# Kernel optimization log

Measured on AMD Instinct MI355X. Metric: run time of the kernel, lower is better.

## Reference

```python
import jax, jax.numpy as jnp
import numpy as np

# Sizes (see init_kwargs / shape_source)
N = 65536      # total points
B = 8          # batch elements
PPB = N // B   # points per batch element (8192, divisible by WS -> no padding)
D = 256        # d_model
H = 8          # nhead
DH = D // H
L = 4          # num_layers
FF = 2048      # torch TransformerEncoderLayer default dim_feedforward
RES = 128      # resolution (coordinate range / embedding table size)
BITS = 7       # ceil(log2(RES)); higher bits of morton loop are zero
WS = 128       # window_size
EPS = 1e-5     # LayerNorm eps


def setup_inputs() -> dict:
    key = jax.random.key(0)
    ks = jax.random.split(key, 16)
    s = 0.02
    batch_col = (jnp.arange(N) // PPB).astype(jnp.int32)
    xyz = jax.random.randint(ks[0], (N, 3), 0, RES, dtype=jnp.int32)
    coords = jnp.concatenate([batch_col[:, None], xyz], axis=1)
    features = jax.random.normal(ks[1], (N, D), jnp.float32)
    inp = {
        'coords': coords,
        'features': features,
        # learned positional embedding tables
        'pe_x': jax.random.normal(ks[2], (RES, D), jnp.float32) * s,
        'pe_y': jax.random.normal(ks[3], (RES, D), jnp.float32) * s,
        'pe_z': jax.random.normal(ks[4], (RES, D), jnp.float32) * s,
        'pe_s': jax.random.normal(ks[5], (RES, D), jnp.float32) * s,
        # stacked transformer encoder layer params (torch post-norm layer)
        'Wqkv': jax.random.normal(ks[6], (L, 3 * D, D), jnp.float32) * s,
        'bqkv': jnp.zeros((L, 3 * D), jnp.float32),
        'Wo': jax.random.normal(ks[7], (L, D, D), jnp.float32) * s,
        'bo': jnp.zeros((L, D), jnp.float32),
        'W1': jax.random.normal(ks[8], (L, FF, D), jnp.float32) * s,
        'b1': jnp.zeros((L, FF), jnp.float32),
        'W2': jax.random.normal(ks[9], (L, D, FF), jnp.float32) * s,
        'b2': jnp.zeros((L, D), jnp.float32),
        'g1': jnp.ones((L, D), jnp.float32),
        'be1': jnp.zeros((L, D), jnp.float32),
        'g2': jnp.ones((L, D), jnp.float32),
        'be2': jnp.zeros((L, D), jnp.float32),
    }
    return inp


def _morton_key(coords):
    # interleave bits of x,y,z (z lowest), prefix with batch index so batch order is preserved
    x, y, z = coords[:, 1], coords[:, 2], coords[:, 3]
    m = jnp.zeros_like(x)
    for i in range(BITS):
        m = m | (((x >> i) & 1) << (3 * i + 2)) \
              | (((y >> i) & 1) << (3 * i + 1)) \
              | (((z >> i) & 1) << (3 * i))
    return coords[:, 0] * (1 << (3 * BITS)) + m


def _ln(x, g, b):
    mu = jnp.mean(x, axis=-1, keepdims=True)
    var = jnp.mean(jnp.square(x - mu), axis=-1, keepdims=True)
    return (x - mu) * jax.lax.rsqrt(var + EPS) * g + b


def _encoder(x, params):
    # x: [Wn, WS, D]; torch TransformerEncoderLayer, post-norm, relu, no dropout (eval)
    scale = float(DH) ** -0.5

    def layer(h, p):
        Wqkv, bqkv, Wo, bo, W1, b1, W2, b2, g1, be1, g2, be2 = p
        Wn = h.shape[0]
        qkv = h @ Wqkv.T + bqkv                      # [Wn, WS, 3D]
        q, k, v = jnp.split(qkv, 3, axis=-1)
        q = q.reshape(Wn, WS, H, DH)
        k = k.reshape(Wn, WS, H, DH)
        v = v.reshape(Wn, WS, H, DH)
        att = jax.nn.softmax(jnp.einsum('wqhd,wkhd->whqk', q, k) * scale, axis=-1)
        o = jnp.einsum('whqk,wkhd->wqhd', att, v).reshape(Wn, WS, D) @ Wo.T + bo
        h = _ln(h + o, g1, be1)
        ff = jax.nn.relu(h @ W1.T + b1) @ W2.T + b2
        h = _ln(h + ff, g2, be2)
        return h, None

    x, _ = jax.lax.scan(layer, x, params)
    return x


def reference(coords, features, pe_x, pe_y, pe_z, pe_s,
              Wqkv, bqkv, Wo, bo, W1, b1, W2, b2, g1, be1, g2, be2):
    # 1) Morton sort (stable, batch-major)
    idx = jnp.argsort(_morton_key(coords))
    sc = coords[idx]
    sf = features[idx]
    # 2) learned positional encoding (stride = 1)
    pe = pe_x[sc[:, 1]] + pe_y[sc[:, 2]] + pe_z[sc[:, 3]] + pe_s[1]
    x = sf + pe
    # 3) window split: PPB % WS == 0, interval == 1 -> exact tiling, no padding
    x = x.reshape(-1, WS, D)                          # [Wn, WS, D]
    # 4) transformer encoder over windows
    x = _encoder(x, (Wqkv, bqkv, Wo, bo, W1, b1, W2, b2, g1, be1, g2, be2))
    # 5) gather back (all masks True -> simple reshape); output in sorted order
    return x.reshape(N, D)
```

## Files before the change

### kernel.cpp

```cpp
#include <hip/hip_runtime.h>

typedef unsigned int u32;
typedef unsigned short u16;

#define NPTS 65536
#define DMODEL 256
#define NHEAD 8
#define DHEAD 32
#define NLAYER 4
#define FFDIM 2048
#define WSIZE 128
#define LNEPS 1e-5f
#define RG 256

#define KSTR 36
#define VSTR 132
#define PSTR 132

typedef __attribute__((ext_vector_type(8))) short short8;
typedef __attribute__((ext_vector_type(4))) float floatx4;

__device__ __forceinline__ float bf2f(u16 v) {
    u32 u = ((u32)v) << 16;
    float f;
    __builtin_memcpy(&f, &u, 4);
    return f;
}
__device__ __forceinline__ u16 f2bf(float f) {
    u32 u;
    __builtin_memcpy(&u, &f, 4);
    u32 r = (u + 0x7fffu + ((u >> 16) & 1u)) >> 16;
    return (u16)r;
}

__device__ __forceinline__ void gl_lds16(const void* g, void* l) {
    __builtin_amdgcn_global_load_lds((const __attribute__((address_space(1))) u32*)g,
                                     (__attribute__((address_space(3))) u32*)l, 16, 0, 0);
}

__global__ __launch_bounds__(256) void morton_kernel(const int* __restrict__ coords,
                                                     u32* __restrict__ key, u32* __restrict__ val) {
    int i = blockIdx.x * 256 + threadIdx.x;
    int b = coords[4 * i + 0];
    int x = coords[4 * i + 1];
    int y = coords[4 * i + 2];
    int z = coords[4 * i + 3];
    u32 m = 0;
#pragma unroll
    for (int t = 0; t < 7; ++t) {
        m |= ((u32)((x >> t) & 1) << (3 * t + 2)) | ((u32)((y >> t) & 1) << (3 * t + 1)) |
             ((u32)((z >> t) & 1) << (3 * t));
    }
    key[i] = ((u32)b << 21) | m;
    val[i] = (u32)i;
}

__global__ __launch_bounds__(256) void hist_kernel(const u32* __restrict__ key, u32* __restrict__ ghist,
                                                   int shift) {
    __shared__ u32 h[256];
    int tid = threadIdx.x;
    h[tid] = 0;
    __syncthreads();
    u32 k = key[blockIdx.x * 256 + tid];
    atomicAdd(&h[(k >> shift) & 255u], 1u);
    __syncthreads();
    ghist[(size_t)tid * RG + blockIdx.x] = h[tid];
}

__global__ __launch_bounds__(256) void scan_up(u32* __restrict__ g, u32* __restrict__ aux) {
    __shared__ u32 wsum[4];
    int tid = threadIdx.x;
    int lane = tid & 63;
    int wave = tid >> 6;
    size_t base = (size_t)blockIdx.x * 1024 + (size_t)tid * 4;
    uint4 v = *(const uint4*)(g + base);
    u32 s = v.x + v.y + v.z + v.w;
    u32 inc = s;
#pragma unroll
    for (int off = 1; off < 64; off <<= 1) {
        u32 u = __shfl_up(inc, off, 64);
        if (lane >= off) inc += u;
    }
    if (lane == 63) wsum[wave] = inc;
    __syncthreads();
    u32 woff = 0;
    for (int w = 0; w < wave; ++w) woff += wsum[w];
    u32 excl = woff + inc - s;
    uint4 o;
    o.x = excl;
    o.y = excl + v.x;
    o.z = excl + v.x + v.y;
    o.w = excl + v.x + v.y + v.z;
    *(uint4*)(g + base) = o;
    if (tid == 255) aux[blockIdx.x] = woff + inc;
}

__global__ __launch_bounds__(256) void scatter_kernel(const u32* __restrict__ keyin, const u32* __restrict__ valin,
                                                      u32* __restrict__ keyout, u32* __restrict__ valout,
                                                      const u32* __restrict__ ghist, const u32* __restrict__ aux,
                                                      int shift) {
    __shared__ u32 whist[4][256];
    __shared__ u32 apre[64];
    int tid = threadIdx.x;
    int lane = tid & 63;
    int wave = tid >> 6;
    uint4 z = {0u, 0u, 0u, 0u};
    ((uint4*)&whist[0][0])[tid] = z;
    if (tid < 64) {
        u32 a = aux[tid];
        u32 inc = a;
#pragma unroll
        for (int off = 1; off < 64; off <<= 1) {
            u32 u = __shfl_up(inc, off, 64);
            if (lane >= off) inc += u;
        }
        apre[tid] = inc - a;
    }
    int gi = blockIdx.x * 256 + tid;
    u32 k = keyin[gi];
    u32 v = valin[gi];
    u32 b = (k >> shift) & 255u;
    __syncthreads();
    unsigned long long m = ~0ull;
#pragma unroll
    for (int bit = 0; bit < 8; ++bit) {
        unsigned long long bb = __ballot((int)((b >> bit) & 1u));
        m &= ((b >> bit) & 1u) ? bb : ~bb;
    }
    unsigned long long below = (lane == 0) ? 0ull : (m & ((1ull << lane) - 1ull));
    int rlane = __popcll(below);
    int cnt = __popcll(m);
    if (rlane == 0) whist[wave][b] = (u32)cnt;
    __syncthreads();
    u32 rank = (u32)rlane;
    for (int w = 0; w < wave; ++w) rank += whist[w][b];
    u32 e = b * (u32)RG + blockIdx.x;
    u32 dst = ghist[e] + apre[e >> 10] + rank;
    keyout[dst] = k;
    valout[dst] = v;
}

__global__ __launch_bounds__(256) void cvt_bf16_kernel(const float* __restrict__ in, u16* __restrict__ out, int n) {
    int i = blockIdx.x * 256 + threadIdx.x;
    if (i < n) out[i] = f2bf(in[i]);
}

template <bool HF32>
__global__ __launch_bounds__(256) void gather_pe_kernel(const u32* __restrict__ idx, const int* __restrict__ coords,
                                                        const float* __restrict__ feat,
                                                        const float* __restrict__ pex, const float* __restrict__ pey,
                                                        const float* __restrict__ pez, const float* __restrict__ pes,
                                                        float* __restrict__ h, u16* __restrict__ xb) {
    int row = blockIdx.x * 4 + (threadIdx.x >> 6);
    int lane = threadIdx.x & 63;
    int src = (int)idx[row];
    int cx = coords[4 * src + 1];
    int cy = coords[4 * src + 2];
    int cz = coords[4 * src + 3];
    int c = lane * 4;
    float4 f = *(const float4*)(feat + (size_t)src * DMODEL + c);
    float4 px = *(const float4*)(pex + (size_t)cx * DMODEL + c);
    float4 py = *(const float4*)(pey + (size_t)cy * DMODEL + c);
    float4 pz = *(const float4*)(pez + (size_t)cz * DMODEL + c);
    float4 ps = *(const float4*)(pes + (size_t)1 * DMODEL + c);
    float4 r;
    r.x = f.x + px.x + py.x + pz.x + ps.x;
    r.y = f.y + px.y + py.y + pz.y + ps.y;
    r.z = f.z + px.z + py.z + pz.z + ps.z;
    r.w = f.w + px.w + py.w + pz.w + ps.w;
    if (HF32) *(float4*)(h + (size_t)row * DMODEL + c) = r;
    ushort4 o;
    o.x = f2bf(r.x);
    o.y = f2bf(r.y);
    o.z = f2bf(r.z);
    o.w = f2bf(r.w);
    *(ushort4*)(xb + (size_t)row * DMODEL + c) = o;
}

template <bool RELU, bool BF16OUT>
__global__ __launch_bounds__(256, 5) void gemm_bt(const u16* __restrict__ A, const u16* __restrict__ W,
                                                  const float* __restrict__ bias, void* __restrict__ Cout,
                                                  int M, int O, int K) {
    __shared__ __align__(16) u16 lA[2 * 128 * 32];
    __shared__ __align__(16) u16 lB[2 * 128 * 32];
    const int tid = threadIdx.x;
    const int lane = tid & 63;
    const int wave = tid >> 6;
    const int wr = wave >> 1;
    const int wc = wave & 1;
    const int quad = lane >> 4;
    const int l16 = lane & 15;
    const int kz = blockIdx.z;
    const int Kpart = K / (int)gridDim.z;
    const size_t row0 = (size_t)blockIdx.x * 128;
    const size_t col0 = (size_t)blockIdx.y * 128;
    floatx4 acc[4][4] = {};

    const int r0 = tid >> 2;
    const int sg0 = (tid & 3) ^ ((r0 >> 1) & 3);
    const u16* pA = A + (row0 + r0) * (size_t)K + (size_t)kz * Kpart + (sg0 << 3);
    const u16* pW = W + (col0 + r0) * (size_t)K + (size_t)kz * Kpart + (sg0 << 3);
    const size_t rstep = (size_t)64 * K;
    const int oA = tid * 8;

    const int nt = Kpart >> 5;
    gl_lds16(pA, lA + oA);
    gl_lds16(pA + rstep, lA + oA + 2048);
    gl_lds16(pW, lB + oA);
    gl_lds16(pW + rstep, lB + oA + 2048);
    pA += 32;
    pW += 32;

    const int sx = (quad ^ ((l16 >> 1) & 3)) << 3;
    const int rdA = (wr * 64 + l16) * 32 + sx;
    const int rdB = (wc * 64 + l16) * 32 + sx;
    int buf = 0;
    for (int t = 0; t < nt; ++t) {
        if (t + 1 < nt) {
            const int nb = (buf ^ 1) * 4096;
            gl_lds16(pA, lA + nb + oA);
            gl_lds16(pA + rstep, lA + nb + oA + 2048);
            gl_lds16(pW, lB + nb + oA);
            gl_lds16(pW + rstep, lB + nb + oA + 2048);
            pA += 32;
            pW += 32;
            asm volatile("s_waitcnt vmcnt(4)" ::: "memory");
        } else {
            asm volatile("s_waitcnt vmcnt(0)" ::: "memory");
        }
        __builtin_amdgcn_s_barrier();
        const u16* la = lA + buf * 4096 + rdA;
        const u16* lb = lB + buf * 4096 + rdB;
        short8 af[4], bf[4];
#pragma unroll
        for (int r = 0; r < 4; ++r) af[r] = *(const short8*)(la + r * 512);
#pragma unroll
        for (int c = 0; c < 4; ++c) bf[c] = *(const short8*)(lb + c * 512);
#pragma unroll
        for (int r = 0; r < 4; ++r)
#pragma unroll
            for (int c = 0; c < 4; ++c)
                acc[r][c] = __builtin_amdgcn_mfma_f32_16x16x32_bf16(af[r], bf[c], acc[r][c], 0, 0, 0);
        if (t + 1 < nt) __builtin_amdgcn_s_barrier();
        buf ^= 1;
    }

    float* Cf = (float*)Cout + (size_t)kz * ((size_t)M * O);
#pragma unroll
    for (int r = 0; r < 4; ++r) {
#pragma unroll
        for (int c = 0; c < 4; ++c) {
            size_t col = col0 + wc * 64 + c * 16 + l16;
            float bv = (kz == 0) ? bias[col] : 0.f;
#pragma unroll
            for (int reg = 0; reg < 4; ++reg) {
                size_t row = row0 + wr * 64 + r * 16 + quad * 4 + reg;
                float v = acc[r][c][reg] + bv;
                if (RELU) v = fmaxf(v, 0.f);
                if (BF16OUT)
                    ((u16*)Cout)[row * O + col] = f2bf(v);
                else
                    Cf[row * O + col] = v;
            }
        }
    }
}

__global__ __launch_bounds__(128) void attn_kernel(const u16* __restrict__ qkv, u16* __restrict__ outb) {
    const int wh = blockIdx.x;
    const int w = wh >> 3;
    const int h = wh & 7;
    const int tid = threadIdx.x;
    const int wave = tid >> 6;
    const int lane = tid & 63;
    const int quad = lane >> 4;
    const int l16 = lane & 15;
    __shared__ __align__(16) u16 lK[128 * KSTR];
    __shared__ __align__(16) u16 lVt[32 * VSTR];
    __shared__ __align__(16) u16 lP[128 * PSTR];
    const u16* base = qkv + (size_t)w * WSIZE * (3 * DMODEL);

    {
        const u16* krow = base + (size_t)tid * (3 * DMODEL) + DMODEL + h * DHEAD;
        const u16* vrow = base + (size_t)tid * (3 * DMODEL) + 2 * DMODEL + h * DHEAD;
#pragma unroll
        for (int p = 0; p < 4; ++p)
            *(short8*)&lK[tid * KSTR + p * 8] = *(const short8*)(krow + p * 8);
        u16 varr[32];
#pragma unroll
        for (int p = 0; p < 4; ++p)
            *(short8*)&varr[p * 8] = *(const short8*)(vrow + p * 8);
#pragma unroll
        for (int d = 0; d < DHEAD; ++d) lVt[d * VSTR + tid] = varr[d];
    }
    short8 af[4];
#pragma unroll
    for (int mi = 0; mi < 4; ++mi)
        af[mi] = *(const short8*)(base + (size_t)(wave * 64 + mi * 16 + l16) * (3 * DMODEL) + h * DHEAD + quad * 8);
    __syncthreads();

    floatx4 acc[4][8] = {};
#pragma unroll
    for (int ni = 0; ni < 8; ++ni) {
        short8 bk = *(const short8*)&lK[(ni * 16 + l16) * KSTR + quad * 8];
#pragma unroll
        for (int mi = 0; mi < 4; ++mi)
            acc[mi][ni] = __builtin_amdgcn_mfma_f32_16x16x32_bf16(af[mi], bk, acc[mi][ni], 0, 0, 0);
    }

    const float scale = 0.17677669529663687f;
    float inv[4][4];
#pragma unroll
    for (int mi = 0; mi < 4; ++mi) {
#pragma unroll
        for (int reg = 0; reg < 4; ++reg) {
            float m = acc[mi][0][reg];
#pragma unroll
            for (int ni = 1; ni < 8; ++ni) m = fmaxf(m, acc[mi][ni][reg]);
            m = fmaxf(m, __shfl_xor(m, 1, 64));
            m = fmaxf(m, __shfl_xor(m, 2, 64));
            m = fmaxf(m, __shfl_xor(m, 4, 64));
            m = fmaxf(m, __shfl_xor(m, 8, 64));
            float e[8];
            float sum = 0.f;
#pragma unroll
            for (int ni = 0; ni < 8; ++ni) {
                e[ni] = __expf((acc[mi][ni][reg] - m) * scale);
                sum += e[ni];
            }
            sum += __shfl_xor(sum, 1, 64);
            sum += __shfl_xor(sum, 2, 64);
            sum += __shfl_xor(sum, 4, 64);
            sum += __shfl_xor(sum, 8, 64);
            inv[mi][reg] = 1.f / sum;
            int row = wave * 64 + mi * 16 + quad * 4 + reg;
#pragma unroll
            for (int ni = 0; ni < 8; ++ni) lP[row * PSTR + ni * 16 + l16] = f2bf(e[ni]);
        }
    }

    floatx4 acc2[4][2] = {};
#pragma unroll
    for (int kt = 0; kt < 4; ++kt) {
        short8 pa[4];
#pragma unroll
        for (int mi = 0; mi < 4; ++mi)
            pa[mi] = *(const short8*)&lP[(wave * 64 + mi * 16 + l16) * PSTR + kt * 32 + quad * 8];
#pragma unroll
        for (int c = 0; c < 2; ++c) {
            short8 bv = *(const short8*)&lVt[(c * 16 + l16) * VSTR + kt * 32 + quad * 8];
#pragma unroll
            for (int mi = 0; mi < 4; ++mi)
                acc2[mi][c] = __builtin_amdgcn_mfma_f32_16x16x32_bf16(pa[mi], bv, acc2[mi][c], 0, 0, 0);
        }
    }

#pragma unroll
    for (int mi = 0; mi < 4; ++mi) {
#pragma unroll
        for (int c = 0; c < 2; ++c) {
#pragma unroll
            for (int reg = 0; reg < 4; ++reg) {
                int row = wave * 64 + mi * 16 + quad * 4 + reg;
                outb[(size_t)(w * WSIZE + row) * DMODEL + h * DHEAD + c * 16 + l16] =
                    f2bf(acc2[mi][c][reg] * inv[mi][reg]);
            }
        }
    }
}

template <bool HF32, bool OUTF32, int NS>
__global__ __launch_bounds__(256) void resid_ln_kernel(const void* __restrict__ hin, const float* __restrict__ delta,
                                                       const float* __restrict__ g, const float* __restrict__ b,
                                                       float* __restrict__ hout, void* __restrict__ nout,
                                                       size_t dstride) {
    int row = blockIdx.x * 4 + (threadIdx.x >> 6);
    int lane = threadIdx.x & 63;
    int c = lane * 4;
    float4 x;
    if (HF32) {
        x = *(const float4*)((const float*)hin + (size_t)row * DMODEL + c);
    } else {
        ushort4 hv = *(const ushort4*)((const u16*)hin + (size_t)row * DMODEL + c);
        x.x = bf2f(hv.x);
        x.y = bf2f(hv.y);
        x.z = bf2f(hv.z);
        x.w = bf2f(hv.w);
    }
    float4 d = *(const float4*)(delta + (size_t)row * DMODEL + c);
    if (NS == 2) {
        float4 d2 = *(const float4*)(delta + dstride + (size_t)row * DMODEL + c);
        d.x += d2.x;
        d.y += d2.y;
        d.z += d2.z;
        d.w += d2.w;
    }
    x.x += d.x;
    x.y += d.y;
    x.z += d.z;
    x.w += d.w;
    float s = x.x + x.y + x.z + x.w;
#pragma unroll
    for (int off = 32; off > 0; off >>= 1) s += __shfl_xor(s, off, 64);
    float mu = s * (1.f / 256.f);
    float d0 = x.x - mu, d1 = x.y - mu, d2 = x.z - mu, d3 = x.w - mu;
    float vs = d0 * d0 + d1 * d1 + d2 * d2 + d3 * d3;
#pragma unroll
    for (int off = 32; off > 0; off >>= 1) vs += __shfl_xor(vs, off, 64);
    float rs = rsqrtf(vs * (1.f / 256.f) + LNEPS);
    float4 gg = *(const float4*)(g + c);
    float4 bb = *(const float4*)(b + c);
    float4 y;
    y.x = d0 * rs * gg.x + bb.x;
    y.y = d1 * rs * gg.y + bb.y;
    y.z = d2 * rs * gg.z + bb.z;
    y.w = d3 * rs * gg.w + bb.w;
    if (HF32) *(float4*)(hout + (size_t)row * DMODEL + c) = y;
    if (OUTF32) {
        *(float4*)((float*)nout + (size_t)row * DMODEL + c) = y;
    } else {
        ushort4 o;
        o.x = f2bf(y.x);
        o.y = f2bf(y.y);
        o.z = f2bf(y.z);
        o.w = f2bf(y.w);
        *(ushort4*)((u16*)nout + (size_t)row * DMODEL + c) = o;
    }
}

extern "C" void kernel_launch(void* const* d_in, const int* in_sizes, int n_in,
                              void* d_out, int out_size, void* d_ws, size_t ws_size,
                              hipStream_t stream) {
    (void)in_sizes;
    (void)n_in;
    (void)out_size;
    const int* coords = (const int*)d_in[0];
    const float* feat = (const float*)d_in[1];
    const float* pex = (const float*)d_in[2];
    const float* pey = (const float*)d_in[3];
    const float* pez = (const float*)d_in[4];
    const float* pes = (const float*)d_in[5];
    const float* Wqkv = (const float*)d_in[6];
    const float* bqkv = (const float*)d_in[7];
    const float* Wo = (const float*)d_in[8];
    const float* bo = (const float*)d_in[9];
    const float* W1 = (const float*)d_in[10];
    const float* b1 = (const float*)d_in[11];
    const float* W2 = (const float*)d_in[12];
    const float* b2 = (const float*)d_in[13];
    const float* g1 = (const float*)d_in[14];
    const float* be1 = (const float*)d_in[15];
    const float* g2 = (const float*)d_in[16];
    const float* be2 = (const float*)d_in[17];

    auto al = [](size_t x) { return (x + 255) & ~(size_t)255; };
    const size_t sortB = 4 * al((size_t)NPTS * 4) + al((size_t)256 * RG * 4) + 256;
    const size_t wqkvB = al((size_t)NLAYER * 3 * DMODEL * DMODEL * 2);
    const size_t woB = al((size_t)NLAYER * DMODEL * DMODEL * 2);
    const size_t w1B = al((size_t)NLAYER * FFDIM * DMODEL * 2);
    const size_t w2B = al((size_t)NLAYER * DMODEL * FFDIM * 2);
    const size_t wB = wqkvB + woB + w1B + w2B;
    const size_t xbB = al((size_t)NPTS * DMODEL * 2);
    const size_t hB = al((size_t)NPTS * DMODEL * 4);

    int CH = 0, KSP = 1;
    bool modeA = true;
    for (int ch = 65536; ch >= 128 && !CH; ch >>= 1) {
        for (int ksp = 2; ksp >= 1; --ksp) {
            size_t need = sortB + wB + xbB + hB + al((size_t)ch * 4096) + al((size_t)ch * 1024 * ksp) + 65536;
            if (need <= ws_size) { CH = ch; KSP = ksp; modeA = true; break; }
        }
    }
    if (!CH) {
        for (int ch = 65536; ch >= 128 && !CH; ch >>= 1) {
            for (int ksp = 2; ksp >= 1; --ksp) {
                size_t need = sortB + wB + xbB + al((size_t)ch * 4096) + al((size_t)ch * 1024 * ksp) + 65536;
                if (need <= ws_size) { CH = ch; KSP = ksp; modeA = false; break; }
            }
        }
    }
    if (!CH) { CH = 128; KSP = 1; modeA = false; }

    char* ws = (char*)d_ws;
    size_t off = 0;
    auto alloc = [&](size_t bytes) -> void* {
        void* p = ws + off;
        off += al(bytes);
        return p;
    };
    u32* key0 = (u32*)alloc(NPTS * 4);
    u32* val0 = (u32*)alloc(NPTS * 4);
    u32* key1 = (u32*)alloc(NPTS * 4);
    u32* val1 = (u32*)alloc(NPTS * 4);
    u32* ghist = (u32*)alloc(256 * RG * 4);
    u32* aux = (u32*)alloc(64 * 4);
    u16* wqkv_b = (u16*)alloc((size_t)NLAYER * 3 * DMODEL * DMODEL * 2);
    u16* wo_b = (u16*)alloc((size_t)NLAYER * DMODEL * DMODEL * 2);
    u16* w1_b = (u16*)alloc((size_t)NLAYER * FFDIM * DMODEL * 2);
    u16* w2_b = (u16*)alloc((size_t)NLAYER * DMODEL * FFDIM * 2);
    u16* xb = (u16*)alloc((size_t)NPTS * DMODEL * 2);
    float* h = modeA ? (float*)alloc((size_t)NPTS * DMODEL * 4) : nullptr;
    u16* scratch1 = (u16*)alloc((size_t)CH * 4096);
    float* tmpc = (float*)alloc((size_t)CH * 1024 * KSP);
    const size_t dstride = (size_t)CH * DMODEL;

    morton_kernel<<<NPTS / 256, 256, 0, stream>>>(coords, key0, val0);

    u32 *ki = key0, *vi = val0, *ko = key1, *vo = val1;
    for (int p = 0; p < 3; ++p) {
        hist_kernel<<<RG, 256, 0, stream>>>(ki, ghist, p * 8);
        scan_up<<<64, 256, 0, stream>>>(ghist, aux);
        scatter_kernel<<<RG, 256, 0, stream>>>(ki, vi, ko, vo, ghist, aux, p * 8);
        u32* t;
        t = ki; ki = ko; ko = t;
        t = vi; vi = vo; vo = t;
    }
    const u32* idx = vi;

    cvt_bf16_kernel<<<(NLAYER * 3 * DMODEL * DMODEL) / 256, 256, 0, stream>>>(Wqkv, wqkv_b, NLAYER * 3 * DMODEL * DMODEL);
    cvt_bf16_kernel<<<(NLAYER * DMODEL * DMODEL) / 256, 256, 0, stream>>>(Wo, wo_b, NLAYER * DMODEL * DMODEL);
    cvt_bf16_kernel<<<(NLAYER * FFDIM * DMODEL) / 256, 256, 0, stream>>>(W1, w1_b, NLAYER * FFDIM * DMODEL);
    cvt_bf16_kernel<<<(NLAYER * DMODEL * FFDIM) / 256, 256, 0, stream>>>(W2, w2_b, NLAYER * DMODEL * FFDIM);

    if (modeA)
        gather_pe_kernel<true><<<NPTS / 4, 256, 0, stream>>>(idx, coords, feat, pex, pey, pez, pes, h, xb);
    else
        gather_pe_kernel<false><<<NPTS / 4, 256, 0, stream>>>(idx, coords, feat, pex, pey, pez, pes, nullptr, xb);

    const int nch = NPTS / CH;
    u16* qkvc = scratch1;
    u16* attoutc = scratch1 + (size_t)CH * 768;
    u16* midc = scratch1;
    for (int l = 0; l < NLAYER; ++l) {
        for (int c = 0; c < nch; ++c) {
            u16* xc = xb + (size_t)c * CH * DMODEL;
            float* hc = modeA ? h + (size_t)c * CH * DMODEL : nullptr;
            gemm_bt<false, true><<<dim3(CH / 128, (3 * DMODEL) / 128), 256, 0, stream>>>(
                xc, wqkv_b + (size_t)l * 3 * DMODEL * DMODEL, bqkv + (size_t)l * 3 * DMODEL, qkvc,
                CH, 3 * DMODEL, DMODEL);
            attn_kernel<<<(CH / WSIZE) * NHEAD, 128, 0, stream>>>(qkvc, attoutc);
            gemm_bt<false, false><<<dim3(CH / 128, DMODEL / 128), 256, 0, stream>>>(
                attoutc, wo_b + (size_t)l * DMODEL * DMODEL, bo + (size_t)l * DMODEL, tmpc,
                CH, DMODEL, DMODEL);
            if (modeA)
                resid_ln_kernel<true, false, 1><<<CH / 4, 256, 0, stream>>>(hc, tmpc, g1 + (size_t)l * DMODEL,
                                                                            be1 + (size_t)l * DMODEL, hc, xc, dstride);
            else
                resid_ln_kernel<false, false, 1><<<CH / 4, 256, 0, stream>>>(xc, tmpc, g1 + (size_t)l * DMODEL,
                                                                             be1 + (size_t)l * DMODEL, nullptr, xc, dstride);
            gemm_bt<true, true><<<dim3(CH / 128, FFDIM / 128), 256, 0, stream>>>(
                xc, w1_b + (size_t)l * FFDIM * DMODEL, b1 + (size_t)l * FFDIM, midc,
                CH, FFDIM, DMODEL);
            gemm_bt<false, false><<<dim3(CH / 128, DMODEL / 128, KSP), 256, 0, stream>>>(
                midc, w2_b + (size_t)l * DMODEL * FFDIM, b2 + (size_t)l * DMODEL, tmpc,
                CH, DMODEL, FFDIM);
            bool last = (l == NLAYER - 1);
            void* outc = last ? (void*)((float*)d_out + (size_t)c * CH * DMODEL) : (void*)xc;
            if (modeA) {
                if (last) {
                    if (KSP == 2)
                        resid_ln_kernel<true, true, 2><<<CH / 4, 256, 0, stream>>>(hc, tmpc, g2 + (size_t)l * DMODEL,
                                                                                   be2 + (size_t)l * DMODEL, hc, outc, dstride);
                    else
                        resid_ln_kernel<true, true, 1><<<CH / 4, 256, 0, stream>>>(hc, tmpc, g2 + (size_t)l * DMODEL,
                                                                                   be2 + (size_t)l * DMODEL, hc, outc, dstride);
                } else {
                    if (KSP == 2)
                        resid_ln_kernel<true, false, 2><<<CH / 4, 256, 0, stream>>>(hc, tmpc, g2 + (size_t)l * DMODEL,
                                                                                    be2 + (size_t)l * DMODEL, hc, outc, dstride);
                    else
                        resid_ln_kernel<true, false, 1><<<CH / 4, 256, 0, stream>>>(hc, tmpc, g2 + (size_t)l * DMODEL,
                                                                                    be2 + (size_t)l * DMODEL, hc, outc, dstride);
                }
            } else {
                if (last) {
                    if (KSP == 2)
                        resid_ln_kernel<false, true, 2><<<CH / 4, 256, 0, stream>>>(xc, tmpc, g2 + (size_t)l * DMODEL,
                                                                                    be2 + (size_t)l * DMODEL, nullptr, outc, dstride);
                    else
                        resid_ln_kernel<false, true, 1><<<CH / 4, 256, 0, stream>>>(xc, tmpc, g2 + (size_t)l * DMODEL,
                                                                                    be2 + (size_t)l * DMODEL, nullptr, outc, dstride);
                } else {
                    if (KSP == 2)
                        resid_ln_kernel<false, false, 2><<<CH / 4, 256, 0, stream>>>(xc, tmpc, g2 + (size_t)l * DMODEL,
                                                                                     be2 + (size_t)l * DMODEL, nullptr, outc, dstride);
                    else
                        resid_ln_kernel<false, false, 1><<<CH / 4, 256, 0, stream>>>(xc, tmpc, g2 + (size_t)l * DMODEL,
                                                                                     be2 + (size_t)l * DMODEL, nullptr, outc, dstride);
                }
            }
        }
    }
}
```

Measured before the change: 2.388 ms.

## Add wide-tile W1 GEMM, split FFN into halves, fuse histogram and weight casts

Adds a dedicated FFN-up GEMM with 128x256 tiles and double-buffered LDS, which gives more MFMA work per A-tile load. The FFN now runs on two half-chunks so the intermediate buffer shrinks to half its size, and the W2 split-K output stride is passed in explicitly. Separately, the first radix-sort histogram is folded into the morton kernel and the four weight-conversion launches are merged into one. The larger tile uses more registers and allows fewer resident blocks, and halving the FFN doubles its launch count.

Measured after the change: 2.214 ms. 1.08x faster.

```diff
diff --git a/kernel.cpp b/kernel.cpp
--- a/kernel.cpp
+++ b/kernel.cpp
@@ -39,8 +39,12 @@
 }
 
 __global__ __launch_bounds__(256) void morton_kernel(const int* __restrict__ coords,
-                                                     u32* __restrict__ key, u32* __restrict__ val) {
-    int i = blockIdx.x * 256 + threadIdx.x;
+                                                     u32* __restrict__ key, u32* __restrict__ val,
+                                                     u32* __restrict__ ghist) {
+    __shared__ u32 hh[256];
+    int tid = threadIdx.x;
+    hh[tid] = 0;
+    int i = blockIdx.x * 256 + tid;
     int b = coords[4 * i + 0];
     int x = coords[4 * i + 1];
     int y = coords[4 * i + 2];
@@ -51,8 +55,13 @@
         m |= ((u32)((x >> t) & 1) << (3 * t + 2)) | ((u32)((y >> t) & 1) << (3 * t + 1)) |
              ((u32)((z >> t) & 1) << (3 * t));
     }
-    key[i] = ((u32)b << 21) | m;
+    u32 k = ((u32)b << 21) | m;
+    key[i] = k;
     val[i] = (u32)i;
+    __syncthreads();
+    atomicAdd(&hh[k & 255u], 1u);
+    __syncthreads();
+    ghist[(size_t)tid * RG + blockIdx.x] = hh[tid];
 }
 
 __global__ __launch_bounds__(256) void hist_kernel(const u32* __restrict__ key, u32* __restrict__ ghist,
@@ -140,9 +149,18 @@
     valout[dst] = v;
 }
 
-__global__ __launch_bounds__(256) void cvt_bf16_kernel(const float* __restrict__ in, u16* __restrict__ out, int n) {
+__global__ __launch_bounds__(256) void cvt_all_kernel(const float* __restrict__ s1, u16* __restrict__ d1, int n1,
+                                                      const float* __restrict__ s2, u16* __restrict__ d2, int n2,
+                                                      const float* __restrict__ s3, u16* __restrict__ d3, int n3,
+                                                      const float* __restrict__ s4, u16* __restrict__ d4, int n4) {
     int i = blockIdx.x * 256 + threadIdx.x;
-    if (i < n) out[i] = f2bf(in[i]);
+    if (i < n1) { d1[i] = f2bf(s1[i]); return; }
+    i -= n1;
+    if (i < n2) { d2[i] = f2bf(s2[i]); return; }
+    i -= n2;
+    if (i < n3) { d3[i] = f2bf(s3[i]); return; }
+    i -= n3;
+    if (i < n4) d4[i] = f2bf(s4[i]);
 }
 
 template <bool HF32>
@@ -180,7 +198,7 @@
 template <bool RELU, bool BF16OUT>
 __global__ __launch_bounds__(256, 5) void gemm_bt(const u16* __restrict__ A, const u16* __restrict__ W,
                                                   const float* __restrict__ bias, void* __restrict__ Cout,
-                                                  int M, int O, int K) {
+                                                  int M, int O, int K, size_t sz) {
     __shared__ __align__(16) u16 lA[2 * 128 * 32];
     __shared__ __align__(16) u16 lB[2 * 128 * 32];
     const int tid = threadIdx.x;
@@ -245,7 +263,7 @@
         buf ^= 1;
     }
 
-    float* Cf = (float*)Cout + (size_t)kz * ((size_t)M * O);
+    float* Cf = (float*)Cout + (size_t)kz * sz;
 #pragma unroll
     for (int r = 0; r < 4; ++r) {
 #pragma unroll
@@ -261,6 +279,92 @@
                     ((u16*)Cout)[row * O + col] = f2bf(v);
                 else
                     Cf[row * O + col] = v;
+            }
+        }
+    }
+}
+
+__global__ __launch_bounds__(256, 2) void gemm_w1(const u16* __restrict__ A, const u16* __restrict__ W,
+                                                  const float* __restrict__ bias, u16* __restrict__ Cout,
+                                                  int O, int K) {
+    __shared__ __align__(16) u16 lA[2 * 128 * 32];
+    __shared__ __align__(16) u16 lB[2 * 256 * 32];
+    const int tid = threadIdx.x;
+    const int lane = tid & 63;
+    const int wave = tid >> 6;
+    const int wr = wave >> 1;
+    const int wc = wave & 1;
+    const int quad = lane >> 4;
+    const int l16 = lane & 15;
+    const size_t row0 = (size_t)blockIdx.x * 128;
+    const size_t col0 = (size_t)blockIdx.y * 256;
+    floatx4 acc[4][8] = {};
+
+    const int r0 = tid >> 2;
+    const int sg0 = (tid & 3) ^ ((r0 >> 1) & 3);
+    const u16* pA = A + (row0 + r0) * (size_t)K + (sg0 << 3);
+    const u16* pW = W + (col0 + r0) * (size_t)K + (sg0 << 3);
+    const size_t rstep = (size_t)64 * K;
+    const int oA = tid * 8;
+
+    const int nt = K >> 5;
+    gl_lds16(pA, lA + oA);
+    gl_lds16(pA + rstep, lA + oA + 2048);
+    gl_lds16(pW, lB + oA);
+    gl_lds16(pW + rstep, lB + oA + 2048);
+    gl_lds16(pW + 2 * rstep, lB + oA + 4096);
+    gl_lds16(pW + 3 * rstep, lB + oA + 6144);
+    pA += 32;
+    pW += 32;
+
+    const int sx = (quad ^ ((l16 >> 1) & 3)) << 3;
+    const int rdA = (wr * 64 + l16) * 32 + sx;
+    const int rdB = (wc * 128 + l16) * 32 + sx;
+    int buf = 0;
+    for (int t = 0; t < nt; ++t) {
+        if (t + 1 < nt) {
+            const int na = (buf ^ 1) * 4096;
+            const int nb = (buf ^ 1) * 8192;
+            gl_lds16(pA, lA + na + oA);
+            gl_lds16(pA + rstep, lA + na + oA + 2048);
+            gl_lds16(pW, lB + nb + oA);
+            gl_lds16(pW + rstep, lB + nb + oA + 2048);
+            gl_lds16(pW + 2 * rstep, lB + nb + oA + 4096);
+            gl_lds16(pW + 3 * rstep, lB + nb + oA + 6144);
+            pA += 32;
+            pW += 32;
+            asm volatile("s_waitcnt vmcnt(6)" ::: "memory");
+        } else {
+            asm volatile("s_waitcnt vmcnt(0)" ::: "memory");
+        }
+        __builtin_amdgcn_s_barrier();
+        const u16* la = lA + buf * 4096 + rdA;
+        const u16* lb = lB + buf * 8192 + rdB;
+        short8 af[4], bf[8];
+#pragma unroll
+        for (int r = 0; r < 4; ++r) af[r] = *(const short8*)(la + r * 512);
+#pragma unroll
+        for (int c = 0; c < 8; ++c) bf[c] = *(const short8*)(lb + c * 512);
+#pragma unroll
+        for (int r = 0; r < 4; ++r)
+#pragma unroll
+            for (int c = 0; c < 8; ++c)
+                acc[r][c] = __builtin_amdgcn_mfma_f32_16x16x32_bf16(af[r], bf[c], acc[r][c], 0, 0, 0);
+        if (t + 1 < nt) __builtin_amdgcn_s_barrier();
+        buf ^= 1;
+    }
+
+#pragma unroll
+    for (int r = 0; r < 4; ++r) {
+#pragma unroll
+        for (int c = 0; c < 8; ++c) {
+            size_t col = col0 + wc * 128 + c * 16 + l16;
+            float bv = bias[col];
+#pragma unroll
+            for (int reg = 0; reg < 4; ++reg) {
+                size_t row = row0 + wr * 64 + r * 16 + quad * 4 + reg;
+                float v = fmaxf(acc[r][c][reg] + bv, 0.f);
+                Cout[row * O + col] = f2bf(v);
             }
         }
     }
@@ -465,21 +569,21 @@
 
     int CH = 0, KSP = 1;
     bool modeA = true;
-    for (int ch = 65536; ch >= 128 && !CH; ch >>= 1) {
+    for (int ch = 65536; ch >= 256 && !CH; ch >>= 1) {
         for (int ksp = 2; ksp >= 1; --ksp) {
-            size_t need = sortB + wB + xbB + hB + al((size_t)ch * 4096) + al((size_t)ch * 1024 * ksp) + 65536;
+            size_t need = sortB + wB + xbB + hB + al((size_t)ch * 2048) + al((size_t)ch * 1024 * ksp) + 65536;
             if (need <= ws_size) { CH = ch; KSP = ksp; modeA = true; break; }
         }
     }
     if (!CH) {
-        for (int ch = 65536; ch >= 128 && !CH; ch >>= 1) {
+        for (int ch = 65536; ch >= 256 && !CH; ch >>= 1) {
             for (int ksp = 2; ksp >= 1; --ksp) {
-                size_t need = sortB + wB + xbB + al((size_t)ch * 4096) + al((size_t)ch * 1024 * ksp) + 65536;
+                size_t need = sortB + wB + xbB + al((size_t)ch * 2048) + al((size_t)ch * 1024 * ksp) + 65536;
                 if (need <= ws_size) { CH = ch; KSP = ksp; modeA = false; break; }
             }
         }
     }
-    if (!CH) { CH = 128; KSP = 1; modeA = false; }
+    if (!CH) { CH = 256; KSP = 1; modeA = false; }
 
     char* ws = (char*)d_ws;
     size_t off = 0;
@@ -500,15 +604,15 @@
     u16* w2_b = (u16*)alloc((size_t)NLAYER * DMODEL * FFDIM * 2);
     u16* xb = (u16*)alloc((size_t)NPTS * DMODEL * 2);
     float* h = modeA ? (float*)alloc((size_t)NPTS * DMODEL * 4) : nullptr;
-    u16* scratch1 = (u16*)alloc((size_t)CH * 4096);
+    u16* scratch1 = (u16*)alloc((size_t)CH * 2048);
     float* tmpc = (float*)alloc((size_t)CH * 1024 * KSP);
     const size_t dstride = (size_t)CH * DMODEL;
 
-    morton_kernel<<<NPTS / 256, 256, 0, stream>>>(coords, key0, val0);
+    morton_kernel<<<NPTS / 256, 256, 0, stream>>>(coords, key0, val0, ghist);
 
     u32 *ki = key0, *vi = val0, *ko = key1, *vo = val1;
     for (int p = 0; p < 3; ++p) {
-        hist_kernel<<<RG, 256, 0, stream>>>(ki, ghist, p * 8);
+        if (p > 0) hist_kernel<<<RG, 256, 0, stream>>>(ki, ghist, p * 8);
         scan_up<<<64, 256, 0, stream>>>(ghist, aux);
         scatter_kernel<<<RG, 256, 0, stream>>>(ki, vi, ko, vo, ghist, aux, p * 8);
         u32* t;
@@ -517,10 +621,14 @@
     }
     const u32* idx = vi;
 
-    cvt_bf16_kernel<<<(NLAYER * 3 * DMODEL * DMODEL) / 256, 256, 0, stream>>>(Wqkv, wqkv_b, NLAYER * 3 * DMODEL * DMODEL);
-    cvt_bf16_kernel<<<(NLAYER * DMODEL * DMODEL) / 256, 256, 0, stream>>>(Wo, wo_b, NLAYER * DMODEL * DMODEL);
-    cvt_bf16_kernel<<<(NLAYER * FFDIM * DMODEL) / 256, 256, 0, stream>>>(W1, w1_b, NLAYER * FFDIM * DMODEL);
-    cvt_bf16_kernel<<<(NLAYER * DMODEL * FFDIM) / 256, 256, 0, stream>>>(W2, w2_b, NLAYER * DMODEL * FFDIM);
+    {
+        const int n1 = NLAYER * 3 * DMODEL * DMODEL;
+        const int n2 = NLAYER * DMODEL * DMODEL;
+        const int n3 = NLAYER * FFDIM * DMODEL;
+        const int n4 = NLAYER * DMODEL * FFDIM;
+        cvt_all_kernel<<<(n1 + n2 + n3 + n4) / 256, 256, 0, stream>>>(Wqkv, wqkv_b, n1, Wo, wo_b, n2,
+                                                                      W1, w1_b, n3, W2, w2_b, n4);
+    }
 
     if (modeA)
         gather_pe_kernel<true><<<NPTS / 4, 256, 0, stream>>>(idx, coords, feat, pex, pey, pez, pes, h, xb);
@@ -537,23 +645,26 @@
             float* hc = modeA ? h + (size_t)c * CH * DMODEL : nullptr;
             gemm_bt<false, true><<<dim3(CH / 128, (3 * DMODEL) / 128), 256, 0, stream>>>(
                 xc, wqkv_b + (size_t)l * 3 * DMODEL * DMODEL, bqkv + (size_t)l * 3 * DMODEL, qkvc,
-                CH, 3 * DMODEL, DMODEL);
+                CH, 3 * DMODEL, DMODEL, 0);
             attn_kernel<<<(CH / WSIZE) * NHEAD, 128, 0, stream>>>(qkvc, attoutc);
             gemm_bt<false, false><<<dim3(CH / 128, DMODEL / 128), 256, 0, stream>>>(
                 attoutc, wo_b + (size_t)l * DMODEL * DMODEL, bo + (size_t)l * DMODEL, tmpc,
-                CH, DMODEL, DMODEL);
+                CH, DMODEL, DMODEL, 0);
             if (modeA)
                 resid_ln_kernel<true, false, 1><<<CH / 4, 256, 0, stream>>>(hc, tmpc, g1 + (size_t)l * DMODEL,
                                                                             be1 + (size_t)l * DMODEL, hc, xc, dstride);
             else
                 resid_ln_kernel<false, false, 1><<<CH / 4, 256, 0, stream>>>(xc, tmpc, g1 + (size_t)l * DMODEL,
                                                                              be1 + (size_t)l * DMODEL, nullptr, xc, dstride);
-            gemm_bt<true, true><<<dim3(CH / 128, FFDIM / 128), 256, 0, stream>>>(
-                xc, w1_b + (size_t)l * FFDIM * DMODEL, b1 + (size_t)l * FFDIM, midc,
-                CH, FFDIM, DMODEL);
-            gemm_bt<false, false><<<dim3(CH / 128, DMODEL / 128, KSP), 256, 0, stream>>>(
-                midc, w2_b + (size_t)l * DMODEL * FFDIM, b2 + (size_t)l * DMODEL, tmpc,
-                CH, DMODEL, FFDIM);
+            const int MH = CH / 2;
+            for (int hf = 0; hf < 2; ++hf) {
+                const u16* xh = xc + (size_t)hf * MH * DMODEL;
+                gemm_w1<<<dim3(MH / 128, FFDIM / 256), 256, 0, stream>>>(
+                    xh, w1_b + (size_t)l * FFDIM * DMODEL, b1 + (size_t)l * FFDIM, midc, FFDIM, DMODEL);
+                gemm_bt<false, false><<<dim3(MH / 128, DMODEL / 128, KSP), 256, 0, stream>>>(
+                    midc, w2_b + (size_t)l * DMODEL * FFDIM, b2 + (size_t)l * DMODEL,
+                    tmpc + (size_t)hf * MH * DMODEL, MH, DMODEL, FFDIM, dstride);
+            }
             bool last = (l == NLAYER - 1);
             void* outc = last ? (void*)((float*)d_out + (size_t)c * CH * DMODEL) : (void*)xc;
             if (modeA) {
```
